# Kernel optimization log

Measured on AMD Instinct MI355X. Metric: run time of the kernel, lower is better.

The kernel has to match this reference:

```python
import jax, jax.numpy as jnp
import numpy as np

IN_F, OUT_F = 256, 256
GRID_SIZE, SPLINE_ORDER = 5, 3
SPLINE_TERMS = GRID_SIZE + SPLINE_ORDER  # 8
PADE_EPS = 1e-4
SHARPNESS = 50.0


def build_grid():
    h = 2.0 / GRID_SIZE  # grid_range (-1, 1)
    g = np.arange(-SPLINE_ORDER, GRID_SIZE + SPLINE_ORDER + 1, dtype=np.float32) * h - 1.0
    return jnp.asarray(np.broadcast_to(g, (IN_F, g.shape[0])).copy())  # [in, 12]


def b_splines(x, grid):
    # x: [B, in], grid: [in, G] -> bases: [B, in, spline_terms]
    xg = x[..., None]  # [B, in, 1]
    g = grid  # broadcasts as [1, in, G]
    bases = ((xg >= g[..., :-1]) & (xg < g[..., 1:])).astype(x.dtype)
    for k in range(1, SPLINE_ORDER + 1):
        left = (xg - g[..., :-(k + 1)]) / (g[..., k:-1] - g[..., :-(k + 1)] + 1e-8)
        right = (g[..., k + 1:] - xg) / (g[..., k + 1:] - g[..., 1:-k] + 1e-8)
        bases = left * bases[..., :-1] + right * bases[..., 1:]
    return bases


def setup_inputs() -> dict:
    key = jax.random.key(0)
    ks = jax.random.split(key, 8)
    B = 4096
    return {
        'x': jax.random.normal(ks[0], (B, IN_F), jnp.float32),
        'base_weight': jax.random.normal(ks[1], (OUT_F, IN_F), jnp.float32) * 0.05,
        'num_spline_weight': jax.random.normal(ks[2], (OUT_F, IN_F, SPLINE_TERMS), jnp.float32) * 0.1,
        'den_spline_weight': jax.random.normal(ks[3], (OUT_F, IN_F, SPLINE_TERMS), jnp.float32) * 0.1,
        'heaviside_bias': jax.random.normal(ks[4], (OUT_F, IN_F), jnp.float32) * 0.1,
        'heaviside_weight': jax.random.normal(ks[5], (OUT_F, IN_F), jnp.float32) * 0.1,
        'l2_den_weight': jax.random.normal(ks[6], (OUT_F, IN_F), jnp.float32) * 0.01,
        'prod_den_weight': jax.random.normal(ks[7], (OUT_F, IN_F), jnp.float32) * 0.01,
        'grid': build_grid(),
    }


def reference(x, base_weight, num_spline_weight, den_spline_weight, heaviside_bias,
              heaviside_weight, l2_den_weight, prod_den_weight, grid):
    act = jax.nn.silu(x)  # base_activation = SiLU
    base_out = jnp.einsum('bi,oi->bo', act, base_weight)
    sb = b_splines(x, grid)  # [B, in, K]
    num_spline = jnp.einsum('bik,oik->boi', sb, num_spline_weight)  # [B, out, in]
    x_diff = x[:, None, :] - heaviside_bias  # [B, out, in]
    heaviside_out = jax.nn.sigmoid(SHARPNESS * x_diff) * heaviside_weight
    numerator = num_spline + heaviside_out
    den_spline = jnp.einsum('bik,oik->boi', sb, den_spline_weight)
    l2_sq = jnp.sum(x * x, axis=-1)[:, None, None]  # [B, 1, 1]
    prod_val = jnp.prod(x, axis=-1)[:, None, None]  # [B, 1, 1]
    denominator = 1.0 + den_spline + l2_sq * l2_den_weight + prod_val * prod_den_weight
    den_safe = jax.nn.softplus(denominator) + PADE_EPS
    pade_out = jnp.sum(numerator / den_safe, axis=-1)  # reduce over in
    return base_out + pade_out
```

## Files before the change

kernel.cpp:

```cpp
#include <hip/hip_runtime.h>


#define IN_F 256
#define OUT_F 256
#define B_TOTAL 4096
#define NWAVE 4
#define NS 4

constexpr float L2E = 1.4426950408889634f;
constexpr float LN2 = 0.6931471805599453f;

typedef _Float16 f16x8 __attribute__((ext_vector_type(8)));
typedef float    f32x16 __attribute__((ext_vector_type(16)));

__device__ __forceinline__ float fast_exp2(float a) { return __builtin_amdgcn_exp2f(a); }
__device__ __forceinline__ float fast_log2(float a) { return __builtin_amdgcn_logf(a); }
__device__ __forceinline__ float fast_rcp(float a)  { return __builtin_amdgcn_rcpf(a); }


__global__ __launch_bounds__(256)
void prep3(const float* __restrict__ bw, const float* __restrict__ nw,
           const float* __restrict__ dw, const float* __restrict__ hb,
           const float* __restrict__ hw, const float* __restrict__ lw,
           const float* __restrict__ pw, const float* __restrict__ x,
           f16x8* __restrict__ sbpk, float* __restrict__ ex,
           _Float16* __restrict__ silu2,
           _Float16* __restrict__ bwp,
           f16x8* __restrict__ bfN, f16x8* __restrict__ bfD,
           float2* __restrict__ misc2,
           float* __restrict__ l2s, float* __restrict__ prs,
           float* __restrict__ out, int out_n)
{
    if (blockIdx.x < 1024) {
        __shared__ float xs[64][17];
        __shared__ __align__(16) _Float16 sil[2][64][16];
        const int bt = blockIdx.x >> 4;
        const int it = blockIdx.x & 15;
        const int b0 = bt * 64;
        const int i0 = it * 16;
        {
            const int rr = threadIdx.x >> 2;
            const int c4 = (threadIdx.x & 3) * 4;
            const float4 v = *reinterpret_cast<const float4*>(
                x + (size_t)(b0 + rr) * IN_F + i0 + c4);
            xs[rr][c4] = v.x; xs[rr][c4 + 1] = v.y;
            xs[rr][c4 + 2] = v.z; xs[rr][c4 + 3] = v.w;
        }
        __syncthreads();
        const int bl = threadIdx.x & 63;
        const int ig = threadIdx.x >> 6;
        #pragma unroll
        for (int k = 0; k < 4; ++k) {
            const int il = ig * 4 + k;
            const int i = i0 + il;
            const float xv = xs[bl][il];
            ex[(size_t)i * B_TOTAL + b0 + bl] =
                fast_exp2(fminf(-50.0f * L2E * xv, 58.0f));
            const float sl = xv * fast_rcp(1.0f + fast_exp2(-L2E * xv));
            const _Float16 sH = (_Float16)sl;
            sil[0][bl][il] = sH;
            sil[1][bl][il] = (_Float16)(sl - (float)sH);
            const float tt = (xv + 2.2f) * 2.5f;
            const float sf = floorf(tt);
            const float u  = tt - sf;
            const float u2 = u * u;
            const float u3 = u2 * u;
            const float om = 1.0f - u;
            const float W0 = om * om * om * (1.0f / 6.0f);
            const float W1 = fmaf(3.0f, u3, fmaf(-6.0f, u2, 4.0f)) * (1.0f / 6.0f);
            const float W2 = fmaf(-3.0f, u3, fmaf(3.0f, u2, fmaf(3.0f, u, 1.0f))) * (1.0f / 6.0f);
            const float W3 = u3 * (1.0f / 6.0f);
            const int  siq = (int)sf;
            f16x8 sb8;
            #pragma unroll
            for (int j = 0; j < 8; ++j) {
                float v = 0.f;
                v = (siq == j + 3) ? W0 : v;
                v = (siq == j + 2) ? W1 : v;
                v = (siq == j + 1) ? W2 : v;
                v = (siq == j    ) ? W3 : v;
                sb8[j] = (_Float16)v;
            }
            sbpk[(size_t)i * B_TOTAL + b0 + bl] = sb8;
        }
        __syncthreads();
        {
            const int hl = threadIdx.x >> 7;
            const int b2 = (threadIdx.x >> 1) & 63;
            const int ch = threadIdx.x & 1;
            const f16x8 v = *reinterpret_cast<const f16x8*>(&sil[hl][b2][ch * 8]);
            *reinterpret_cast<f16x8*>(
                silu2 + (size_t)hl * B_TOTAL * IN_F +
                (size_t)(b0 + b2) * IN_F + i0 + ch * 8) = v;
        }
    } else if (blockIdx.x < 1280) {
        const int i = blockIdx.x - 1024;
        const int o = threadIdx.x;
        const int oi = o * IN_F + i;
        const float* n8 = nw + (size_t)oi * 8;
        const float* d8 = dw + (size_t)oi * 8;
        f16x8 vhi, vlo, vd;
        #pragma unroll
        for (int k = 0; k < 8; ++k) {
            const float nv = n8[k];
            const _Float16 h = (_Float16)nv;
            vhi[k] = h;
            vlo[k] = (_Float16)(nv - (float)h);
            vd[k]  = (_Float16)d8[k];
        }
        const float lwv = lw[oi], pwv = pw[oi];
        const _Float16 lwh = (_Float16)lwv;
        const _Float16 lwl = (_Float16)(lwv - (float)lwh);
        const _Float16 z0 = (_Float16)0.0f;
        const f16x8 vs = {lwh, lwl, lwh, (_Float16)pwv, (_Float16)1.0f, z0, z0, z0};
        const int ot = o >> 5, ol = o & 31;
        const size_t base = ((size_t)i * 8 + ot) * 64;
        bfN[base + ol]      = vhi;
        bfN[base + 32 + ol] = vlo;
        bfD[base + ol]      = vd;
        bfD[base + 32 + ol] = vs;
        misc2[(size_t)i * OUT_F + o] =
            make_float2(fast_exp2(hb[oi] * (50.0f * L2E)), hw[oi]);
        bwp[(size_t)o * IN_F + i] = (_Float16)bw[oi];
    } else if (blockIdx.x < 1536) {
        const int blk = blockIdx.x - 1280;
        const int wv = threadIdx.x >> 6;
        const int lane = threadIdx.x & 63;
        const int row = blk * NWAVE + wv;
        #pragma unroll
        for (int rr = 0; rr < 4; ++rr) {
            const int r = row * 4 + rr;
            const float* xr = x + (size_t)r * IN_F;
            float pl2 = 0.f, ppr = 1.f;
            #pragma unroll
            for (int c = 0; c < 4; ++c) {
                float xv = xr[c * 64 + lane];
                pl2 = fmaf(xv, xv, pl2);
                ppr *= xv;
            }
            #pragma unroll
            for (int m = 1; m < 64; m <<= 1) {
                pl2 += __shfl_xor(pl2, m);
                ppr *= __shfl_xor(ppr, m);
            }
            if (lane == 0) { l2s[r] = pl2; prs[r] = ppr; }
        }
    } else {
        const size_t base = ((size_t)(blockIdx.x - 1536) * 256 + threadIdx.x) * 4;
        if (base + 4 <= (size_t)out_n)
            *reinterpret_cast<float4*>(out + base) = make_float4(0.f, 0.f, 0.f, 0.f);
    }
}

__global__ __launch_bounds__(256, 5)
void padekan_mfma3(const f16x8* __restrict__ sbpk, const float* __restrict__ ex,
                   const _Float16* __restrict__ silu2, const _Float16* __restrict__ bwp,
                   const f16x8* __restrict__ bfN, const f16x8* __restrict__ bfD,
                   const float2* __restrict__ misc2, const float* __restrict__ l2s,
                   const float* __restrict__ prs, float* __restrict__ out)
{
    __shared__ float red[NS][64][17];

    const int lane = threadIdx.x & 63;
    const int wv = threadIdx.x >> 6;
    const int xcd = blockIdx.x & 7;
    const int r   = blockIdx.x >> 3;
    const int ot  = r >> 5;
    const int btl = (r >> 1) & 15;
    const int ih  = r & 1;
    const int bt  = xcd * 16 + btl;
    const int bl = lane & 31;
    const int hi = lane >> 5;
    const int b0 = bt * 32;
    const int bme = b0 + bl;

    const float l2v = l2s[bme];
    const float prv = prs[bme];
    const _Float16 l2h = (_Float16)l2v;
    const _Float16 l2l = (_Float16)(l2v - (float)l2h);
    const _Float16 z0 = (_Float16)0.0f;
    const f16x8 stat8 = {l2h, l2h, l2l, (_Float16)prv, (_Float16)1.0f, z0, z0, z0};

    const f32x16 zero16 = {};
    f32x16 acc = {};

    const int i0 = ih * 128 + wv * 32;
    #pragma unroll 1
    for (int ii = 0; ii < 32; ++ii) {
        const int i = i0 + ii;

        if ((ii & 7) == 0) {
            const size_t sidx = (size_t)hi * (B_TOTAL * IN_F) + (size_t)bme * IN_F + i;
            const f16x8 sfr = *reinterpret_cast<const f16x8*>(silu2 + sidx);
            const f16x8 wfr = *reinterpret_cast<const f16x8*>(
                bwp + (size_t)(ot * 32 + bl) * IN_F + i);
            acc = __builtin_amdgcn_mfma_f32_32x32x16_f16(sfr, wfr, acc, 0, 0, 0);
        }

        const f16x8 sbv = sbpk[(size_t)i * B_TOTAL + bme];
        const size_t fb = ((size_t)i * 8 + ot) * 64 + lane;
        const f16x8 vbN = bfN[fb];
        const f16x8 vbD = bfD[fb];
        const float2 mi = misc2[(size_t)i * OUT_F + ot * 32 + bl];
        const f16x8 aD = hi ? stat8 : sbv;

        f32x16 cn = __builtin_amdgcn_mfma_f32_32x32x16_f16(sbv, vbN, zero16, 0, 0, 0);
        f32x16 cd = __builtin_amdgcn_mfma_f32_32x32x16_f16(aD, vbD, zero16, 0, 0, 0);

        const float* ep = ex + (size_t)i * B_TOTAL + b0 + hi * 4;
        #pragma unroll
        for (int gq = 0; gq < 4; ++gq) {
            const float4 eA = *reinterpret_cast<const float4*>(ep + gq * 8);
            const float exq[4] = {eA.x, eA.y, eA.z, eA.w};
            #pragma unroll
            for (int j = 0; j < 4; ++j) {
                const int rr_ = gq * 4 + j;
                const float den = cd[rr_];
                const float t1  = fast_exp2(L2E * den);
                const float spe = fmaf(fast_log2(1.0f + t1), LN2, 1e-4f);
                const float q   = fmaf(exq[j], mi.x, 1.0f);
                const float rrv = fast_rcp(q * spe);
                acc[rr_] = fmaf(fmaf(cn[rr_], q, mi.y), rrv, acc[rr_]);
            }
        }
    }

    #pragma unroll
    for (int oo = 0; oo < 16; ++oo) red[wv][lane][oo] = acc[oo];
    __syncthreads();
    #pragma unroll
    for (int e = 0; e < 4; ++e) {
        const int l = threadIdx.x & 63;
        const int rr_ = (threadIdx.x >> 6) + e * 4;
        const float s = (red[0][l][rr_] + red[1][l][rr_]) +
                        (red[2][l][rr_] + red[3][l][rr_]);
        const int row = (rr_ & 3) + 8 * (rr_ >> 2) + 4 * (l >> 5);
        atomicAdd(&out[(size_t)(b0 + row) * OUT_F + ot * 32 + (l & 31)], s);
    }
}


__global__ __launch_bounds__(256)
void prep_mfma(const float* __restrict__ bw, const float* __restrict__ nw,
               const float* __restrict__ dw, const float* __restrict__ hb,
               const float* __restrict__ hw, const float* __restrict__ lw,
               const float* __restrict__ pw, const float* __restrict__ x,
               float* __restrict__ xT, float2* __restrict__ exsi,
               f16x8* __restrict__ bfN, f16x8* __restrict__ bfD,
               float4* __restrict__ misc,
               float* __restrict__ l2s, float* __restrict__ prs)
{
    if (blockIdx.x < 256) {
        const int i = blockIdx.x;
        const int o = threadIdx.x;
        const int oi = o * IN_F + i;
        const float* n8 = nw + (size_t)oi * 8;
        const float* d8 = dw + (size_t)oi * 8;
        f16x8 vhi, vlo, vd;
        #pragma unroll
        for (int k = 0; k < 8; ++k) {
            const float nv = n8[k];
            const _Float16 h = (_Float16)nv;
            vhi[k] = h;
            vlo[k] = (_Float16)(nv - (float)h);
            vd[k]  = (_Float16)d8[k];
        }
        const float lwv = lw[oi], pwv = pw[oi];
        const _Float16 lwh = (_Float16)lwv;
        const _Float16 lwl = (_Float16)(lwv - (float)lwh);
        const _Float16 z0 = (_Float16)0.0f;
        const f16x8 vs = {lwh, lwl, lwh, (_Float16)pwv, (_Float16)1.0f, z0, z0, z0};
        const int ot = o >> 5, ol = o & 31;
        const size_t base = ((size_t)i * 8 + ot) * 64;
        bfN[base + ol]      = vhi;
        bfN[base + 32 + ol] = vlo;
        bfD[base + ol]      = vd;
        bfD[base + 32 + ol] = vs;
        misc[(size_t)i * OUT_F + o] =
            make_float4(fast_exp2(hb[oi] * (50.0f * L2E)), hw[oi], bw[oi], 0.0f);
    } else if (blockIdx.x < 512) {
        __shared__ float t[64][65];
        const int blk = blockIdx.x - 256;
        const int bt = blk >> 2;
        const int it = blk & 3;
        const int c  = threadIdx.x & 63;
        const int r0 = threadIdx.x >> 6;
        #pragma unroll
        for (int rr = 0; rr < 16; ++rr) {
            const int r = r0 * 16 + rr;
            t[r][c] = x[(size_t)(bt * 64 + r) * IN_F + it * 64 + c];
        }
        __syncthreads();
        #pragma unroll
        for (int rr = 0; rr < 16; ++rr) {
            const int r = r0 * 16 + rr;
            const float v = t[c][r];
            const size_t idx = (size_t)(it * 64 + r) * B_TOTAL + bt * 64 + c;
            xT[idx] = v;
            const float exv = fast_exp2(fminf(-50.0f * L2E * v, 58.0f));
            const float sl = v * fast_rcp(1.0f + fast_exp2(-L2E * v));
            exsi[idx] = make_float2(exv, sl);
        }
    } else {
        const int blk = blockIdx.x - 512;
        const int wv = threadIdx.x >> 6;
        const int lane = threadIdx.x & 63;
        const int row = blk * NWAVE + wv;
        #pragma unroll
        for (int rr = 0; rr < 4; ++rr) {
            const int r = row * 4 + rr;
            const float* xr = x + (size_t)r * IN_F;
            float pl2 = 0.f, ppr = 1.f;
            #pragma unroll
            for (int c = 0; c < 4; ++c) {
                float xv = xr[c * 64 + lane];
                pl2 = fmaf(xv, xv, pl2);
                ppr *= xv;
            }
            #pragma unroll
            for (int m = 1; m < 64; m <<= 1) {
                pl2 += __shfl_xor(pl2, m);
                ppr *= __shfl_xor(ppr, m);
            }
            if (lane == 0) { l2s[r] = pl2; prs[r] = ppr; }
        }
    }
}

__global__ __launch_bounds__(256, 4)
void padekan_mfma(const float* __restrict__ xT, const float2* __restrict__ exsi,
                  const f16x8* __restrict__ bfN, const f16x8* __restrict__ bfD,
                  const float4* __restrict__ misc, const float* __restrict__ l2s,
                  const float* __restrict__ prs, const float* __restrict__ grid,
                  float* __restrict__ out)
{
    __shared__ float red[NS][64][17];

    const int lane = threadIdx.x & 63;
    const int wv = threadIdx.x >> 6;
    const int ot = blockIdx.x & 7;
    const int bt = blockIdx.x >> 3;
    const int bl = lane & 31;
    const int hi = lane >> 5;
    const int b0 = bt * 32;

    const float g0 = grid[0];
    const float inv_h = 1.0f / (grid[1] - grid[0]);

    const float l2v = l2s[b0 + bl];
    const float prv = prs[b0 + bl];
    const _Float16 l2h = (_Float16)l2v;
    const _Float16 l2l = (_Float16)(l2v - (float)l2h);
    const _Float16 z0 = (_Float16)0.0f;
    const f16x8 stat8 = {l2h, l2h, l2l, (_Float16)prv, (_Float16)1.0f, z0, z0, z0};

    const f32x16 zero16 = {};
    f32x16 acc = {};

    const int i0 = wv * 64;
    #pragma unroll 1
    for (int ii = 0; ii < 64; ++ii) {
        const int i = i0 + ii;
        const float xv = xT[(size_t)i * B_TOTAL + b0 + bl];

        const float t  = (xv - g0) * inv_h;
        const float sf = floorf(t);
        const float u  = t - sf;
        const float u2 = u * u;
        const float u3 = u2 * u;
        const float om = 1.0f - u;
        const float W0 = om * om * om * (1.0f / 6.0f);
        const float W1 = fmaf(3.0f, u3, fmaf(-6.0f, u2, 4.0f)) * (1.0f / 6.0f);
        const float W2 = fmaf(-3.0f, u3, fmaf(3.0f, u2, fmaf(3.0f, u, 1.0f))) * (1.0f / 6.0f);
        const float W3 = u3 * (1.0f / 6.0f);
        const int  si = (int)sf;

        f16x8 aN;
        #pragma unroll
        for (int j = 0; j < 8; ++j) {
            float v = 0.f;
            v = (si == j + 3) ? W0 : v;
            v = (si == j + 2) ? W1 : v;
            v = (si == j + 1) ? W2 : v;
            v = (si == j    ) ? W3 : v;
            aN[j] = (_Float16)v;
        }
        const f16x8 aD = hi ? stat8 : aN;

        const size_t fb = ((size_t)i * 8 + ot) * 64 + lane;
        const f16x8 vbN = bfN[fb];
        const f16x8 vbD = bfD[fb];
        const float4 mi = misc[(size_t)i * OUT_F + ot * 32 + bl];

        f32x16 cn = __builtin_amdgcn_mfma_f32_32x32x16_f16(aN, vbN, zero16, 0, 0, 0);
        f32x16 cd = __builtin_amdgcn_mfma_f32_32x32x16_f16(aD, vbD, zero16, 0, 0, 0);

        const float2* ep = exsi + (size_t)i * B_TOTAL + b0 + hi * 4;
        #pragma unroll
        for (int gq = 0; gq < 4; ++gq) {
            const float4 eA = *reinterpret_cast<const float4*>(ep + gq * 8);
            const float4 eB = *reinterpret_cast<const float4*>(ep + gq * 8 + 2);
            const float exq[4] = {eA.x, eA.z, eB.x, eB.z};
            const float svq[4] = {eA.y, eA.w, eB.y, eB.w};
            #pragma unroll
            for (int j = 0; j < 4; ++j) {
                const int r = gq * 4 + j;
                const float den = cd[r];
                const float ttv = fast_exp2(-L2E * fabsf(den));
                const float sp  = fmaf(fast_log2(1.0f + ttv), LN2, fmaxf(den, 0.0f));
                const float q   = fmaf(exq[j], mi.x, 1.0f);
                const float rrv = fast_rcp(q * (sp + 1e-4f));
                const float numer = fmaf(cn[r], q, mi.y);
                acc[r] = fmaf(svq[j], mi.z, fmaf(numer, rrv, acc[r]));
            }
        }
    }

    #pragma unroll
    for (int oo = 0; oo < 16; ++oo) red[wv][lane][oo] = acc[oo];
    __syncthreads();
    #pragma unroll
    for (int e = 0; e < 4; ++e) {
        const int l = threadIdx.x & 63;
        const int r = (threadIdx.x >> 6) + e * 4;
        const float s = (red[0][l][r] + red[1][l][r]) + (red[2][l][r] + red[3][l][r]);
        const int row = (r & 3) + 8 * (r >> 2) + 4 * (l >> 5);
        out[(size_t)(b0 + row) * OUT_F + ot * 32 + (l & 31)] = s;
    }
}


__global__ __launch_bounds__(256)
void padekan_fallback(const float* __restrict__ x,  const float* __restrict__ base_w,
                      const float* __restrict__ num_w, const float* __restrict__ den_w,
                      const float* __restrict__ hbias, const float* __restrict__ hweight,
                      const float* __restrict__ l2w, const float* __restrict__ pw,
                      const float* __restrict__ grid, float* __restrict__ out)
{
    const int b = blockIdx.x;
    const int o = threadIdx.x;
    const float g0 = grid[0];
    const float inv_h = 1.0f / (grid[1] - grid[0]);
    const float* xrow = x + (size_t)b * IN_F;
    float l2v = 0.f, prodv = 1.f;
    for (int i = 0; i < IN_F; ++i) { float xv = xrow[i]; l2v = fmaf(xv, xv, l2v); prodv *= xv; }
    float acc = 0.f;
    for (int i = 0; i < IN_F; ++i) {
        const float xv = xrow[i];
        const float t = (xv - g0) * inv_h;
        const float sf = floorf(t);
        const float u = t - sf;
        const float u2 = u * u, u3 = u2 * u, om = 1.0f - u;
        const float W[4] = {om * om * om / 6.0f,
                            fmaf(3.0f, u3, fmaf(-6.0f, u2, 4.0f)) / 6.0f,
                            fmaf(-3.0f, u3, fmaf(3.0f, u2, fmaf(3.0f, u, 1.0f))) / 6.0f,
                            u3 / 6.0f};
        const int si = (int)sf;
        const int oi = o * IN_F + i;
        float num = 0.f, den = fmaf(l2v, l2w[oi], fmaf(prodv, pw[oi], 1.0f));
        #pragma unroll
        for (int w = 0; w < 4; ++w) {
            const int j = si - 3 + w;
            if (j >= 0 && j < 8) {
                num = fmaf(W[w], num_w[(size_t)oi * 8 + j], num);
                den = fmaf(W[w], den_w[(size_t)oi * 8 + j], den);
            }
        }
        float q = fminf(fast_exp2(fminf((hbias[oi] - xv) * (50.0f * L2E), 99.0f)), 1e30f) + 1.0f;
        float tt = fast_exp2(-L2E * fabsf(den));
        float sp = fmaf(fast_log2(1.0f + tt), LN2, fmaxf(den, 0.0f));
        float rr = fast_rcp(q * (sp + 1e-4f));
        float silu_v = xv * fast_rcp(1.0f + fast_exp2(-L2E * xv));
        acc = fmaf(silu_v, base_w[oi], fmaf(fmaf(num, q, hweight[oi]), rr, acc));
    }
    out[(size_t)b * OUT_F + o] = acc;
}

extern "C" void kernel_launch(void* const* d_in, const int* in_sizes, int n_in,
                              void* d_out, int out_size, void* d_ws, size_t ws_size,
                              hipStream_t stream) {
    const float* xp  = (const float*)d_in[0];
    const float* bw  = (const float*)d_in[1];
    const float* nw  = (const float*)d_in[2];
    const float* dw  = (const float*)d_in[3];
    const float* hb  = (const float*)d_in[4];
    const float* hw  = (const float*)d_in[5];
    const float* lw  = (const float*)d_in[6];
    const float* pwt = (const float*)d_in[7];
    const float* gr  = (const float*)d_in[8];
    float* outp = (float*)d_out;

    const size_t sbpk_b = (size_t)IN_F * B_TOTAL * sizeof(f16x8);
    const size_t ex_b   = (size_t)IN_F * B_TOTAL * sizeof(float);
    const size_t si2_b  = (size_t)2 * B_TOTAL * IN_F * sizeof(_Float16);
    const size_t bwp_b  = (size_t)OUT_F * IN_F * sizeof(_Float16);
    const size_t bf_b   = (size_t)IN_F * 8 * 64 * sizeof(f16x8);
    const size_t mi2_b  = (size_t)IN_F * OUT_F * sizeof(float2);
    const size_t st_b   = (size_t)B_TOTAL * 2 * sizeof(float);
    const size_t tier1  = sbpk_b + ex_b + si2_b + bwp_b + 2 * bf_b + mi2_b + st_b;

    const size_t xT_b   = (size_t)B_TOTAL * IN_F * sizeof(float);
    const size_t exsi_b = (size_t)B_TOTAL * IN_F * sizeof(float2);
    const size_t misc_b = (size_t)IN_F * OUT_F * sizeof(float4);
    const size_t tier2  = xT_b + exsi_b + 2 * bf_b + misc_b + st_b;

    dim3 block(256);

    if (ws_size >= tier1) {
        char* p = (char*)d_ws;
        f16x8*     sbpk = (f16x8*)p;      p += sbpk_b;
        float*     exA  = (float*)p;      p += ex_b;
        _Float16*  si2  = (_Float16*)p;   p += si2_b;
        _Float16*  bwp  = (_Float16*)p;   p += bwp_b;
        f16x8*     bfN  = (f16x8*)p;      p += bf_b;
        f16x8*     bfD  = (f16x8*)p;      p += bf_b;
        float2*    mi2  = (float2*)p;     p += mi2_b;
        float*     l2sp = (float*)p;
        float*     prsp = l2sp + B_TOTAL;
        prep3<<<dim3(2560), block, 0, stream>>>(
            bw, nw, dw, hb, hw, lw, pwt, xp, sbpk, exA, si2, bwp, bfN, bfD,
            mi2, l2sp, prsp, outp, out_size);
        padekan_mfma3<<<dim3(2048), block, 0, stream>>>(
            sbpk, exA, si2, bwp, bfN, bfD, mi2, l2sp, prsp, outp);
    } else if (ws_size >= tier2) {
        char* p = (char*)d_ws;
        float*  xT   = (float*)p;            p += xT_b;
        float2* exsi = (float2*)p;           p += exsi_b;
        f16x8*  bfN  = (f16x8*)p;            p += bf_b;
        f16x8*  bfD  = (f16x8*)p;            p += bf_b;
        float4* misc = (float4*)p;           p += misc_b;
        float*  l2sp = (float*)p;
        float*  prsp = l2sp + B_TOTAL;
        prep_mfma<<<dim3(768), block, 0, stream>>>(
            bw, nw, dw, hb, hw, lw, pwt, xp, xT, exsi, bfN, bfD, misc, l2sp, prsp);
        padekan_mfma<<<dim3(1024), block, 0, stream>>>(
            xT, exsi, bfN, bfD, misc, l2sp, prsp, gr, outp);
    } else {
        padekan_fallback<<<dim3(B_TOTAL), dim3(OUT_F), 0, stream>>>(
            xp, bw, nw, dw, hb, hw, lw, pwt, gr, outp);
    }
}
```

Baseline: 197.2 us.

## Fold log2e into denominator weights, split input range across more blocks

```diff
diff --git a/kernel.cpp b/kernel.cpp
--- a/kernel.cpp
+++ b/kernel.cpp
@@ -19,7 +19,7 @@
 
 
 __global__ __launch_bounds__(256)
-void prep3(const float* __restrict__ bw, const float* __restrict__ nw,
+void prep4(const float* __restrict__ bw, const float* __restrict__ nw,
            const float* __restrict__ dw, const float* __restrict__ hb,
            const float* __restrict__ hw, const float* __restrict__ lw,
            const float* __restrict__ pw, const float* __restrict__ x,
@@ -106,13 +106,15 @@
             const _Float16 h = (_Float16)nv;
             vhi[k] = h;
             vlo[k] = (_Float16)(nv - (float)h);
-            vd[k]  = (_Float16)d8[k];
-        }
-        const float lwv = lw[oi], pwv = pw[oi];
+            vd[k]  = (_Float16)(d8[k] * L2E);
+        }
+        const float lwv = lw[oi] * L2E, pwv = pw[oi] * L2E;
         const _Float16 lwh = (_Float16)lwv;
         const _Float16 lwl = (_Float16)(lwv - (float)lwh);
+        const _Float16 cEh = (_Float16)L2E;
+        const _Float16 cEl = (_Float16)(L2E - (float)cEh);
         const _Float16 z0 = (_Float16)0.0f;
-        const f16x8 vs = {lwh, lwl, lwh, (_Float16)pwv, (_Float16)1.0f, z0, z0, z0};
+        const f16x8 vs = {lwh, lwl, lwh, (_Float16)pwv, cEh, cEl, z0, z0};
         const int ot = o >> 5, ol = o & 31;
         const size_t base = ((size_t)i * 8 + ot) * 64;
         bfN[base + ol]      = vhi;
@@ -152,8 +154,8 @@
     }
 }
 
-__global__ __launch_bounds__(256, 5)
-void padekan_mfma3(const f16x8* __restrict__ sbpk, const float* __restrict__ ex,
+__global__ __launch_bounds__(256, 8)
+void padekan_mfma4(const f16x8* __restrict__ sbpk, const float* __restrict__ ex,
                    const _Float16* __restrict__ silu2, const _Float16* __restrict__ bwp,
                    const f16x8* __restrict__ bfN, const f16x8* __restrict__ bfD,
                    const float2* __restrict__ misc2, const float* __restrict__ l2s,
@@ -165,9 +167,9 @@
     const int wv = threadIdx.x >> 6;
     const int xcd = blockIdx.x & 7;
     const int r   = blockIdx.x >> 3;
-    const int ot  = r >> 5;
-    const int btl = (r >> 1) & 15;
-    const int ih  = r & 1;
+    const int ih  = r & 3;
+    const int btl = (r >> 2) & 15;
+    const int ot  = r >> 6;
     const int bt  = xcd * 16 + btl;
     const int bl = lane & 31;
     const int hi = lane >> 5;
@@ -179,49 +181,59 @@
     const _Float16 l2h = (_Float16)l2v;
     const _Float16 l2l = (_Float16)(l2v - (float)l2h);
     const _Float16 z0 = (_Float16)0.0f;
-    const f16x8 stat8 = {l2h, l2h, l2l, (_Float16)prv, (_Float16)1.0f, z0, z0, z0};
+    const _Float16 one = (_Float16)1.0f;
+    const f16x8 stat8 = {l2h, l2h, l2l, (_Float16)prv, one, one, z0, z0};
 
     const f32x16 zero16 = {};
     f32x16 acc = {};
 
-    const int i0 = ih * 128 + wv * 32;
+    const int i0 = ih * 64 + wv * 16;
+
+    const f16x8*   sb_p = sbpk + (size_t)i0 * B_TOTAL + bme;
+    const f16x8*   bn_p = bfN + ((size_t)i0 * 8 + ot) * 64 + lane;
+    const f16x8*   bd_p = bfD + ((size_t)i0 * 8 + ot) * 64 + lane;
+    const float2*  mi_p = misc2 + (size_t)i0 * OUT_F + ot * 32 + bl;
+    const float*   ep   = ex + (size_t)i0 * B_TOTAL + b0 + hi * 4;
+    const _Float16* si_p = silu2 + (size_t)hi * (B_TOTAL * IN_F) + (size_t)bme * IN_F + i0;
+    const _Float16* bw_p = bwp + (size_t)(ot * 32 + bl) * IN_F + i0;
+
     #pragma unroll 1
-    for (int ii = 0; ii < 32; ++ii) {
-        const int i = i0 + ii;
-
-        if ((ii & 7) == 0) {
-            const size_t sidx = (size_t)hi * (B_TOTAL * IN_F) + (size_t)bme * IN_F + i;
-            const f16x8 sfr = *reinterpret_cast<const f16x8*>(silu2 + sidx);
-            const f16x8 wfr = *reinterpret_cast<const f16x8*>(
-                bwp + (size_t)(ot * 32 + bl) * IN_F + i);
+    for (int half = 0; half < 2; ++half) {
+        {
+            const f16x8 sfr = *reinterpret_cast<const f16x8*>(si_p + half * 8);
+            const f16x8 wfr = *reinterpret_cast<const f16x8*>(bw_p + half * 8);
             acc = __builtin_amdgcn_mfma_f32_32x32x16_f16(sfr, wfr, acc, 0, 0, 0);
         }
-
-        const f16x8 sbv = sbpk[(size_t)i * B_TOTAL + bme];
-        const size_t fb = ((size_t)i * 8 + ot) * 64 + lane;
-        const f16x8 vbN = bfN[fb];
-        const f16x8 vbD = bfD[fb];
-        const float2 mi = misc2[(size_t)i * OUT_F + ot * 32 + bl];
-        const f16x8 aD = hi ? stat8 : sbv;
-
-        f32x16 cn = __builtin_amdgcn_mfma_f32_32x32x16_f16(sbv, vbN, zero16, 0, 0, 0);
-        f32x16 cd = __builtin_amdgcn_mfma_f32_32x32x16_f16(aD, vbD, zero16, 0, 0, 0);
-
-        const float* ep = ex + (size_t)i * B_TOTAL + b0 + hi * 4;
-        #pragma unroll
-        for (int gq = 0; gq < 4; ++gq) {
-            const float4 eA = *reinterpret_cast<const float4*>(ep + gq * 8);
-            const float exq[4] = {eA.x, eA.y, eA.z, eA.w};
-            #pragma unroll
-            for (int j = 0; j < 4; ++j) {
-                const int rr_ = gq * 4 + j;
-                const float den = cd[rr_];
-                const float t1  = fast_exp2(L2E * den);
-                const float spe = fmaf(fast_log2(1.0f + t1), LN2, 1e-4f);
-                const float q   = fmaf(exq[j], mi.x, 1.0f);
-                const float rrv = fast_rcp(q * spe);
-                acc[rr_] = fmaf(fmaf(cn[rr_], q, mi.y), rrv, acc[rr_]);
-            }
+        #pragma unroll 1
+        for (int ii = 0; ii < 8; ++ii) {
+            const f16x8 sbv = *sb_p;
+            const f16x8 vbN = *bn_p;
+            const f16x8 vbD = *bd_p;
+            const float2 mi = *mi_p;
+            const f16x8 aD = hi ? stat8 : sbv;
+
+            f32x16 cn = __builtin_amdgcn_mfma_f32_32x32x16_f16(sbv, vbN, zero16, 0, 0, 0);
+            f32x16 cd = __builtin_amdgcn_mfma_f32_32x32x16_f16(aD, vbD, zero16, 0, 0, 0);
+
+            #pragma unroll
+            for (int gq = 0; gq < 4; ++gq) {
+                const float4 eA = *reinterpret_cast<const float4*>(ep + gq * 8);
+                const float exq[4] = {eA.x, eA.y, eA.z, eA.w};
+                #pragma unroll
+                for (int j = 0; j < 4; ++j) {
+                    const int rr_ = gq * 4 + j;
+                    const float t1  = fast_exp2(cd[rr_]);
+                    const float spe = fmaf(fast_log2(1.0f + t1), LN2, 1e-4f);
+                    const float q   = fmaf(exq[j], mi.x, 1.0f);
+                    const float rrv = fast_rcp(q * spe);
+                    acc[rr_] = fmaf(fmaf(cn[rr_], q, mi.y), rrv, acc[rr_]);
+                }
+            }
+            sb_p += B_TOTAL;
+            bn_p += 8 * 64;
+            bd_p += 8 * 64;
+            mi_p += OUT_F;
+            ep   += B_TOTAL;
         }
     }
 
@@ -517,10 +529,10 @@
         float2*    mi2  = (float2*)p;     p += mi2_b;
         float*     l2sp = (float*)p;
         float*     prsp = l2sp + B_TOTAL;
-        prep3<<<dim3(2560), block, 0, stream>>>(
+        prep4<<<dim3(2560), block, 0, stream>>>(
             bw, nw, dw, hb, hw, lw, pwt, xp, sbpk, exA, si2, bwp, bfN, bfD,
             mi2, l2sp, prsp, outp, out_size);
-        padekan_mfma3<<<dim3(2048), block, 0, stream>>>(
+        padekan_mfma4<<<dim3(4096), block, 0, stream>>>(
             sbpk, exA, si2, bwp, bfN, bfD, mi2, l2sp, prsp, outp);
     } else if (ws_size >= tier2) {
         char* p = (char*)d_ws;
```

New measurement: 300.7 us. +52.5%, slower.
